# Kernel tuning notes

Hardware: AMD Instinct MI355X
Metric: run time of the kernel (lower is better)

## Reference

```python
import jax, jax.numpy as jnp
import numpy as np

N_EMBD = 1024
NUM_HEADS = 16
HEAD_SIZE = 64
B, T, T_ENC = 2, 2048, 2048


def setup_inputs() -> dict:
    key = jax.random.key(0)
    k1, k2, k3, k4, k5 = jax.random.split(key, 5)
    scale = 1.0 / np.sqrt(N_EMBD)
    return {
        "x_enc": jax.random.normal(k1, (B, T_ENC, N_EMBD), dtype=jnp.float32),
        "x": jax.random.normal(k2, (B, T, N_EMBD), dtype=jnp.float32),
        "Wk": jax.random.normal(k3, (N_EMBD, NUM_HEADS * HEAD_SIZE), dtype=jnp.float32) * scale,
        "Wq": jax.random.normal(k4, (N_EMBD, NUM_HEADS * HEAD_SIZE), dtype=jnp.float32) * scale,
        "Wv": jax.random.normal(k5, (N_EMBD, NUM_HEADS * HEAD_SIZE), dtype=jnp.float32) * scale,
    }


def reference(x_enc, x, Wk, Wq, Wv):
    b, t, c = x.shape
    _, t_enc, _ = x_enc.shape
    # projections (bias-free linears)
    k = (x_enc @ Wk).reshape(b, t_enc, NUM_HEADS, HEAD_SIZE)  # [B,S,H,D]
    v = (x_enc @ Wv).reshape(b, t_enc, NUM_HEADS, HEAD_SIZE)
    q = (x @ Wq).reshape(b, t, NUM_HEADS, HEAD_SIZE)          # [B,T,H,D]
    # NOTE: original scales by C**-0.5 with C = n_embd (not head_size)
    scale = jnp.asarray(c, x.dtype) ** -0.5
    wei = jnp.einsum("bthd,bshd->bhts", q, k) * scale          # [B,H,T,S]
    wei = jax.nn.softmax(wei, axis=-1)
    out = jnp.einsum("bhts,bshd->bthd", wei, v)                # [B,T,H,D]
    return out
```

## Files before the change

kernel.cpp:

```cpp
#include <hip/hip_runtime.h>
#include <hip/hip_bf16.h>
#include <stdint.h>

#define NE 1024
#define NH 16
#define HD 64
#define BB 2
#define TT 2048
#define MM (BB*TT)

typedef __attribute__((ext_vector_type(8))) short short8;
typedef __attribute__((ext_vector_type(4))) float floatx4;

__device__ __forceinline__ short f2bf(float f) {
    union { float f; uint32_t u; } v; v.f = f;
    uint32_t u = v.u;
    return (short)((u + 0x7fffu + ((u >> 16) & 1u)) >> 16);
}

__device__ __forceinline__ float fast_exp2(float x) {
#if __has_builtin(__builtin_amdgcn_exp2f)
    return __builtin_amdgcn_exp2f(x);
#else
    float r; asm("v_exp_f32 %0, %1" : "=v"(r) : "v"(x)); return r;
#endif
}

__device__ __forceinline__ void gload_lds16(const void* g, void* l) {
    __builtin_amdgcn_global_load_lds((__attribute__((address_space(1))) void*)g,
                                     (__attribute__((address_space(3))) void*)l,
                                     16, 0, 0);
}

__global__ void cvt_bf16(const float* __restrict__ in, short* __restrict__ out, int n8) {
    int i = blockIdx.x * blockDim.x + threadIdx.x;
    if (i >= n8) return;
    const floatx4* p = (const floatx4*)(in + (size_t)i * 8);
    floatx4 a = p[0], b = p[1];
    union { uint32_t u[4]; short8 s; } r;
    asm("v_cvt_pk_bf16_f32 %0, %1, %2" : "=v"(r.u[0]) : "v"(a[0]), "v"(a[1]));
    asm("v_cvt_pk_bf16_f32 %0, %1, %2" : "=v"(r.u[1]) : "v"(a[2]), "v"(a[3]));
    asm("v_cvt_pk_bf16_f32 %0, %1, %2" : "=v"(r.u[2]) : "v"(b[0]), "v"(b[1]));
    asm("v_cvt_pk_bf16_f32 %0, %1, %2" : "=v"(r.u[3]) : "v"(b[2]), "v"(b[3]));
    *(short8*)(out + (size_t)i * 8) = r.s;
}

__global__ void wtrans(const float* __restrict__ Wq, const float* __restrict__ Wk,
                       const float* __restrict__ Wv, short* __restrict__ Wt) {
    __shared__ float t[32][33];
    const float* W = blockIdx.z == 0 ? Wq : (blockIdx.z == 1 ? Wk : Wv);
    short* dst = Wt + (size_t)blockIdx.z * NE * NE;
    int n0 = blockIdx.x * 32, k0 = blockIdx.y * 32;
    int tx = threadIdx.x & 31, ty = threadIdx.x >> 5;
    #pragma unroll
    for (int i = 0; i < 4; i++)
        t[ty * 4 + i][tx] = W[(size_t)(k0 + ty * 4 + i) * NE + n0 + tx];
    __syncthreads();
    #pragma unroll
    for (int i = 0; i < 4; i++)
        dst[(size_t)(n0 + ty * 4 + i) * NE + k0 + tx] = f2bf(t[tx][ty * 4 + i]);
}

__global__ void __launch_bounds__(256) gemm_bt(const short* __restrict__ x_bf,
                                               const short* __restrict__ xenc_bf,
                                               const short* __restrict__ Wt,
                                               short* __restrict__ qkv) {
    __shared__ short sA[128 * 32];
    __shared__ short sB[128 * 32];
    const int z = blockIdx.z;
    const short* A  = (z == 0) ? x_bf : xenc_bf;
    const short* Bt = Wt + (size_t)z * NE * NE;
    short* C = qkv + (size_t)z * MM * NE;
    const float osc = (z == 0) ? 0.04508422f : 1.0f;

    const int tid = threadIdx.x;
    const int lane = tid & 63, wid = tid >> 6;
    const int l15 = lane & 15, lg = lane >> 4;
    const int wr = wid >> 1, wc = wid & 1;
    const int m0 = blockIdx.y * 128, n0 = blockIdx.x * 128;

    const short* gA = A  + (size_t)(m0 + (tid >> 2)) * NE + (tid & 3) * 8;
    const short* gB = Bt + (size_t)(n0 + (tid >> 2)) * NE + (tid & 3) * 8;
    short* lA = sA + wid * 512;
    short* lB = sB + wid * 512;

    floatx4 acc[4][4];
    floatx4 zero = {0.f, 0.f, 0.f, 0.f};
    #pragma unroll
    for (int i = 0; i < 4; i++)
        #pragma unroll
        for (int j = 0; j < 4; j++) acc[i][j] = zero;

    for (int kt = 0; kt < NE; kt += 32) {
        gload_lds16(gA + kt,            lA);
        gload_lds16(gA + 64 * NE + kt,  lA + 2048);
        gload_lds16(gB + kt,            lB);
        gload_lds16(gB + 64 * NE + kt,  lB + 2048);
        __syncthreads();
        short8 af[4], bfr[4];
        #pragma unroll
        for (int i = 0; i < 4; i++) {
            af[i]  = *(const short8*)&sA[(wr * 64 + i * 16 + l15) * 32 + lg * 8];
            bfr[i] = *(const short8*)&sB[(wc * 64 + i * 16 + l15) * 32 + lg * 8];
        }
        #pragma unroll
        for (int i = 0; i < 4; i++)
            #pragma unroll
            for (int j = 0; j < 4; j++)
                acc[i][j] = __builtin_amdgcn_mfma_f32_16x16x32_bf16(af[i], bfr[j], acc[i][j], 0, 0, 0);
        __syncthreads();
    }
    #pragma unroll
    for (int i = 0; i < 4; i++)
        #pragma unroll
        for (int j = 0; j < 4; j++)
            #pragma unroll
            for (int r = 0; r < 4; r++) {
                int row = m0 + wr * 64 + i * 16 + lg * 4 + r;
                int col = n0 + wc * 64 + j * 16 + l15;
                C[(size_t)row * NE + col] = f2bf(acc[i][j][r] * osc);
            }
}

__global__ void vtrans(const short* __restrict__ v, short* __restrict__ vt) {
    __shared__ short t[64][65];
    int s0 = blockIdx.x * 64;
    int bh = blockIdx.y;
    int b = bh >> 4, h = bh & 15;
    int tid = threadIdx.x;
    int c = tid & 63, rr = tid >> 6;
    #pragma unroll
    for (int i = 0; i < 16; i++)
        t[i * 4 + rr][c] = v[(size_t)(b * TT + s0 + i * 4 + rr) * NE + h * HD + c];
    __syncthreads();
    int csw = (c & 35) | (((c >> 4) & 1) << 2) | (((c >> 2) & 3) << 3);
    #pragma unroll
    for (int i = 0; i < 16; i++)
        vt[(size_t)(bh * HD + i * 4 + rr) * TT + s0 + csw] = t[c][i * 4 + rr];
}

__global__ void __launch_bounds__(256, 2) fattn(const short* __restrict__ q,
                                                const short* __restrict__ k,
                                                const short* __restrict__ vt,
                                                float* __restrict__ out) {
    __shared__ short kbuf[3][4096];
    __shared__ short vbuf[3][4096];
    const int tid = threadIdx.x, lane = tid & 63, wid = tid >> 6;
    const int l15 = lane & 15, lg = lane >> 4;
    const int q0 = blockIdx.x * 128 + wid * 32;
    const int bh = blockIdx.y, b = bh >> 4, h = bh & 15;

    short8 qf[2][2];
    #pragma unroll
    for (int qb = 0; qb < 2; qb++) {
        const short* qp = q + (size_t)(b * TT + q0 + qb * 16 + l15) * NE + h * HD + lg * 8;
        qf[qb][0] = *(const short8*)qp;
        qf[qb][1] = *(const short8*)(qp + 32);
    }
    short8 ones;
    #pragma unroll
    for (int j = 0; j < 8; j++) ones[j] = (short)0x3F80;

    floatx4 acc_o[2][4];
    floatx4 acc_l[2];
    floatx4 zero = {0.f, 0.f, 0.f, 0.f};
    floatx4 minus8 = {-8.f, -8.f, -8.f, -8.f};
    #pragma unroll
    for (int qb = 0; qb < 2; qb++) {
        acc_l[qb] = zero;
        #pragma unroll
        for (int db = 0; db < 4; db++) acc_o[qb][db] = zero;
    }

    const char* kgb = (const char*)(k + (size_t)(b * TT) * NE + h * HD);
    const char* vgb = (const char*)(vt + (size_t)bh * HD * TT);
    const int srow = tid >> 3;
    const int ssw  = ((tid & 7) * 16) ^ ((srow & 7) << 4);
    const char* ksrc = kgb + (size_t)srow * (NE * 2) + ssw;
    const char* vsrc = vgb + (size_t)srow * (TT * 2) + ssw;

    const int swz  = (l15 & 7) << 4;
    const int rd0  = l15 * 128 + ((lg * 16) ^ swz);
    const int rd1  = l15 * 128 + ((64 + lg * 16) ^ swz);

#define STAGE(bi, s0v) do { \
    const char* ks_ = ksrc + (size_t)(s0v) * (NE * 2); \
    gload_lds16(ks_,                 &kbuf[bi][wid * 512]); \
    gload_lds16(ks_ + 32 * (NE * 2), &kbuf[bi][wid * 512 + 2048]); \
    const char* vs_ = vsrc + (size_t)(s0v) * 2; \
    gload_lds16(vs_,                 &vbuf[bi][wid * 512]); \
    gload_lds16(vs_ + 32 * (TT * 2), &vbuf[bi][wid * 512 + 2048]); \
} while (0)

#define FATTN_COMPUTE(cur) do { \
    const char* kb = (const char*)kbuf[cur]; \
    const char* vb = (const char*)vbuf[cur]; \
    short8 kf[4][2]; \
    _Pragma("unroll") \
    for (int cb = 0; cb < 4; cb++) { \
        kf[cb][0] = *(const short8*)(kb + cb * 2048 + rd0); \
        kf[cb][1] = *(const short8*)(kb + cb * 2048 + rd1); \
    } \
    floatx4 sacc[2][4]; \
    _Pragma("unroll") \
    for (int qb = 0; qb < 2; qb++) \
        _Pragma("unroll") \
        for (int cb = 0; cb < 4; cb++) sacc[qb][cb] = minus8; \
    __builtin_amdgcn_s_setprio(1); \
    _Pragma("unroll") \
    for (int qb = 0; qb < 2; qb++) \
        _Pragma("unroll") \
        for (int cb = 0; cb < 4; cb++) { \
            sacc[qb][cb] = __builtin_amdgcn_mfma_f32_16x16x32_bf16(kf[cb][0], qf[qb][0], sacc[qb][cb], 0, 0, 0); \
            sacc[qb][cb] = __builtin_amdgcn_mfma_f32_16x16x32_bf16(kf[cb][1], qf[qb][1], sacc[qb][cb], 0, 0, 0); \
        } \
    __builtin_amdgcn_s_setprio(0); \
    short8 vf[2][4]; \
    _Pragma("unroll") \
    for (int db = 0; db < 4; db++) { \
        vf[0][db] = *(const short8*)(vb + db * 2048 + rd0); \
        vf[1][db] = *(const short8*)(vb + db * 2048 + rd1); \
    } \
    short8 paf[2][2]; \
    _Pragma("unroll") \
    for (int qb = 0; qb < 2; qb++) { \
        float pe[16]; \
        _Pragma("unroll") \
        for (int cb = 0; cb < 4; cb++) \
            _Pragma("unroll") \
            for (int r = 0; r < 4; r++) \
                pe[cb * 4 + r] = fast_exp2(sacc[qb][cb][r]); \
        _Pragma("unroll") \
        for (int ks = 0; ks < 2; ks++) { \
            union { uint32_t u[4]; short8 s; } pk_; \
            _Pragma("unroll") \
            for (int j2 = 0; j2 < 4; j2++) \
                asm("v_cvt_pk_bf16_f32 %0, %1, %2" \
                    : "=v"(pk_.u[j2]) \
                    : "v"(pe[ks * 8 + 2 * j2]), "v"(pe[ks * 8 + 2 * j2 + 1])); \
            paf[qb][ks] = pk_.s; \
        } \
    } \
    __builtin_amdgcn_s_setprio(1); \
    _Pragma("unroll") \
    for (int qb = 0; qb < 2; qb++) \
        _Pragma("unroll") \
        for (int ks = 0; ks < 2; ks++) { \
            _Pragma("unroll") \
            for (int db = 0; db < 4; db++) \
                acc_o[qb][db] = __builtin_amdgcn_mfma_f32_16x16x32_bf16(paf[qb][ks], vf[ks][db], acc_o[qb][db], 0, 0, 0); \
            acc_l[qb] = __builtin_amdgcn_mfma_f32_16x16x32_bf16(paf[qb][ks], ones, acc_l[qb], 0, 0, 0); \
        } \
    __builtin_amdgcn_s_setprio(0); \
} while (0)

    STAGE(0, 0);
    STAGE(1, 64);
    for (int t = 0; t < 31; ++t) {
        asm volatile("s_waitcnt vmcnt(4)" ::: "memory");
        __builtin_amdgcn_sched_barrier(0);
        __builtin_amdgcn_s_barrier();
        __builtin_amdgcn_sched_barrier(0);
        if (t < 30) STAGE((t + 2) % 3, (t + 2) * 64);
        FATTN_COMPUTE(t % 3);
    }
    asm volatile("s_waitcnt vmcnt(0)" ::: "memory");
    __builtin_amdgcn_sched_barrier(0);
    __builtin_amdgcn_s_barrier();
    __builtin_amdgcn_sched_barrier(0);
    FATTN_COMPUTE(1);
#undef STAGE
#undef FATTN_COMPUTE

    #pragma unroll
    for (int qb = 0; qb < 2; qb++) {
        #pragma unroll
        for (int r = 0; r < 4; r++) {
            float inv = 1.0f / acc_l[qb][r];
            #pragma unroll
            for (int db = 0; db < 4; db++)
                out[(size_t)(b * TT + q0 + qb * 16 + lg * 4 + r) * NE + h * HD + db * 16 + l15] =
                    acc_o[qb][db][r] * inv;
        }
    }
}

extern "C" void kernel_launch(void* const* d_in, const int* in_sizes, int n_in,
                              void* d_out, int out_size, void* d_ws, size_t ws_size,
                              hipStream_t stream) {
    const float* x_enc = (const float*)d_in[0];
    const float* x     = (const float*)d_in[1];
    const float* Wk    = (const float*)d_in[2];
    const float* Wq    = (const float*)d_in[3];
    const float* Wv    = (const float*)d_in[4];
    float* out = (float*)d_out;

    const size_t SZ = (size_t)MM * NE;
    short* x_bf    = (short*)d_ws;
    short* xenc_bf = x_bf + SZ;
    short* Wt      = xenc_bf + SZ;
    short* qkv     = Wt + 3 * (size_t)NE * NE;
    short* vt      = qkv + 3 * SZ;

    cvt_bf16<<<dim3(2048), dim3(256), 0, stream>>>(x,     x_bf,    (int)(SZ / 8));
    cvt_bf16<<<dim3(2048), dim3(256), 0, stream>>>(x_enc, xenc_bf, (int)(SZ / 8));
    wtrans<<<dim3(32, 32, 3), dim3(256), 0, stream>>>(Wq, Wk, Wv, Wt);
    gemm_bt<<<dim3(8, 32, 3), dim3(256), 0, stream>>>(x_bf, xenc_bf, Wt, qkv);
    vtrans<<<dim3(32, 32), dim3(256), 0, stream>>>(qkv + 2 * SZ, vt);
    fattn<<<dim3(16, 32), dim3(256), 0, stream>>>(qkv, qkv + SZ, vt, out);
}
```

Baseline: 101.6 us.

## Pipeline GEMM with triple-buffered LDS, XCD-aware block mapping, register-prefetch V in attention

Merges the two bf16 conversion kernels into one launch. Gives the projection GEMM a triple-buffered LDS pipeline that loads asynchronously to LDS, raises MFMA priority, and remaps 1D block ids so that neighbouring tiles share an XCD. The attention kernel gets the same XCD-aware remap, drops the V LDS staging in favour of direct global-to-register double-buffered V loads, and prefetches the next K fragments from LDS into registers. The aim is to overlap memory with MFMA work and improve L2 locality, at the cost of more registers and a full vmcnt(0) wait each iteration.

```diff
diff --git a/kernel.cpp b/kernel.cpp
--- a/kernel.cpp
+++ b/kernel.cpp
@@ -32,17 +32,20 @@
                                      16, 0, 0);
 }
 
-__global__ void cvt_bf16(const float* __restrict__ in, short* __restrict__ out, int n8) {
+__global__ void cvt_bf16_2(const float* __restrict__ ina, const float* __restrict__ inb,
+                           short* __restrict__ outa, short* __restrict__ outb, int n8half) {
     int i = blockIdx.x * blockDim.x + threadIdx.x;
-    if (i >= n8) return;
-    const floatx4* p = (const floatx4*)(in + (size_t)i * 8);
+    const float* in; short* out; int j;
+    if (i < n8half) { in = ina; out = outa; j = i; }
+    else            { in = inb; out = outb; j = i - n8half; }
+    const floatx4* p = (const floatx4*)(in + (size_t)j * 8);
     floatx4 a = p[0], b = p[1];
     union { uint32_t u[4]; short8 s; } r;
     asm("v_cvt_pk_bf16_f32 %0, %1, %2" : "=v"(r.u[0]) : "v"(a[0]), "v"(a[1]));
     asm("v_cvt_pk_bf16_f32 %0, %1, %2" : "=v"(r.u[1]) : "v"(a[2]), "v"(a[3]));
     asm("v_cvt_pk_bf16_f32 %0, %1, %2" : "=v"(r.u[2]) : "v"(b[0]), "v"(b[1]));
     asm("v_cvt_pk_bf16_f32 %0, %1, %2" : "=v"(r.u[3]) : "v"(b[2]), "v"(b[3]));
-    *(short8*)(out + (size_t)i * 8) = r.s;
+    *(short8*)(out + (size_t)j * 8) = r.s;
 }
 
 __global__ void wtrans(const float* __restrict__ Wq, const float* __restrict__ Wk,
@@ -65,9 +68,15 @@
                                                const short* __restrict__ xenc_bf,
                                                const short* __restrict__ Wt,
                                                short* __restrict__ qkv) {
-    __shared__ short sA[128 * 32];
-    __shared__ short sB[128 * 32];
-    const int z = blockIdx.z;
+    __shared__ short sA[3][4096];
+    __shared__ short sB[3][4096];
+    const int bid = blockIdx.x;
+    const int xcd = bid & 7, inner = bid >> 3;
+    const int xblk = inner & 7;
+    const int yh = (inner >> 3) & 3;
+    const int z = inner >> 5;
+    const int yblk = xcd + 8 * yh;
+
     const short* A  = (z == 0) ? x_bf : xenc_bf;
     const short* Bt = Wt + (size_t)z * NE * NE;
     short* C = qkv + (size_t)z * MM * NE;
@@ -77,12 +86,10 @@
     const int lane = tid & 63, wid = tid >> 6;
     const int l15 = lane & 15, lg = lane >> 4;
     const int wr = wid >> 1, wc = wid & 1;
-    const int m0 = blockIdx.y * 128, n0 = blockIdx.x * 128;
+    const int m0 = yblk * 128, n0 = xblk * 128;
 
     const short* gA = A  + (size_t)(m0 + (tid >> 2)) * NE + (tid & 3) * 8;
     const short* gB = Bt + (size_t)(n0 + (tid >> 2)) * NE + (tid & 3) * 8;
-    short* lA = sA + wid * 512;
-    short* lB = sB + wid * 512;
 
     floatx4 acc[4][4];
     floatx4 zero = {0.f, 0.f, 0.f, 0.f};
@@ -91,25 +98,47 @@
         #pragma unroll
         for (int j = 0; j < 4; j++) acc[i][j] = zero;
 
-    for (int kt = 0; kt < NE; kt += 32) {
-        gload_lds16(gA + kt,            lA);
-        gload_lds16(gA + 64 * NE + kt,  lA + 2048);
-        gload_lds16(gB + kt,            lB);
-        gload_lds16(gB + 64 * NE + kt,  lB + 2048);
-        __syncthreads();
-        short8 af[4], bfr[4];
-        #pragma unroll
-        for (int i = 0; i < 4; i++) {
-            af[i]  = *(const short8*)&sA[(wr * 64 + i * 16 + l15) * 32 + lg * 8];
-            bfr[i] = *(const short8*)&sB[(wc * 64 + i * 16 + l15) * 32 + lg * 8];
-        }
-        #pragma unroll
-        for (int i = 0; i < 4; i++)
-            #pragma unroll
-            for (int j = 0; j < 4; j++)
-                acc[i][j] = __builtin_amdgcn_mfma_f32_16x16x32_bf16(af[i], bfr[j], acc[i][j], 0, 0, 0);
-        __syncthreads();
-    }
+#define GSTAGE(bi, kt) do { \
+    gload_lds16(gA + (kt),            &sA[bi][wid * 512]); \
+    gload_lds16(gA + 64 * NE + (kt),  &sA[bi][wid * 512 + 2048]); \
+    gload_lds16(gB + (kt),            &sB[bi][wid * 512]); \
+    gload_lds16(gB + 64 * NE + (kt),  &sB[bi][wid * 512 + 2048]); \
+} while (0)
+
+#define GCOMP(cur) do { \
+    short8 af[4], bfr[4]; \
+    _Pragma("unroll") \
+    for (int i = 0; i < 4; i++) { \
+        af[i]  = *(const short8*)&sA[cur][(wr * 64 + i * 16 + l15) * 32 + lg * 8]; \
+        bfr[i] = *(const short8*)&sB[cur][(wc * 64 + i * 16 + l15) * 32 + lg * 8]; \
+    } \
+    __builtin_amdgcn_s_setprio(1); \
+    _Pragma("unroll") \
+    for (int i = 0; i < 4; i++) \
+        _Pragma("unroll") \
+        for (int j = 0; j < 4; j++) \
+            acc[i][j] = __builtin_amdgcn_mfma_f32_16x16x32_bf16(af[i], bfr[j], acc[i][j], 0, 0, 0); \
+    __builtin_amdgcn_s_setprio(0); \
+} while (0)
+
+    GSTAGE(0, 0);
+    GSTAGE(1, 32);
+    for (int t = 0; t < 31; ++t) {
+        asm volatile("s_waitcnt vmcnt(4)" ::: "memory");
+        __builtin_amdgcn_sched_barrier(0);
+        __builtin_amdgcn_s_barrier();
+        __builtin_amdgcn_sched_barrier(0);
+        if (t < 30) GSTAGE((t + 2) % 3, (t + 2) * 32);
+        GCOMP(t % 3);
+    }
+    asm volatile("s_waitcnt vmcnt(0)" ::: "memory");
+    __builtin_amdgcn_sched_barrier(0);
+    __builtin_amdgcn_s_barrier();
+    __builtin_amdgcn_sched_barrier(0);
+    GCOMP(1);
+#undef GSTAGE
+#undef GCOMP
+
     #pragma unroll
     for (int i = 0; i < 4; i++)
         #pragma unroll
@@ -144,11 +173,14 @@
                                                 const short* __restrict__ vt,
                                                 float* __restrict__ out) {
     __shared__ short kbuf[3][4096];
-    __shared__ short vbuf[3][4096];
     const int tid = threadIdx.x, lane = tid & 63, wid = tid >> 6;
     const int l15 = lane & 15, lg = lane >> 4;
-    const int q0 = blockIdx.x * 128 + wid * 32;
-    const int bh = blockIdx.y, b = bh >> 4, h = bh & 15;
+    const int bid = blockIdx.x;
+    const int xcd = bid & 7, rest = bid >> 3;
+    const int qblk = rest & 15;
+    const int bh = xcd + 8 * (rest >> 4);
+    const int b = bh >> 4, h = bh & 15;
+    const int q0 = qblk * 128 + wid * 32;
 
     short8 qf[2][2];
     #pragma unroll
@@ -173,34 +205,36 @@
     }
 
     const char* kgb = (const char*)(k + (size_t)(b * TT) * NE + h * HD);
-    const char* vgb = (const char*)(vt + (size_t)bh * HD * TT);
     const int srow = tid >> 3;
     const int ssw  = ((tid & 7) * 16) ^ ((srow & 7) << 4);
     const char* ksrc = kgb + (size_t)srow * (NE * 2) + ssw;
-    const char* vsrc = vgb + (size_t)srow * (TT * 2) + ssw;
+    const short* vrow = vt + (size_t)(bh * HD + l15) * TT + lg * 8;
 
     const int swz  = (l15 & 7) << 4;
     const int rd0  = l15 * 128 + ((lg * 16) ^ swz);
     const int rd1  = l15 * 128 + ((64 + lg * 16) ^ swz);
 
-#define STAGE(bi, s0v) do { \
+#define KSTAGE(bi, s0v) do { \
     const char* ks_ = ksrc + (size_t)(s0v) * (NE * 2); \
     gload_lds16(ks_,                 &kbuf[bi][wid * 512]); \
     gload_lds16(ks_ + 32 * (NE * 2), &kbuf[bi][wid * 512 + 2048]); \
-    const char* vs_ = vsrc + (size_t)(s0v) * 2; \
-    gload_lds16(vs_,                 &vbuf[bi][wid * 512]); \
-    gload_lds16(vs_ + 32 * (TT * 2), &vbuf[bi][wid * 512 + 2048]); \
-} while (0)
-
-#define FATTN_COMPUTE(cur) do { \
-    const char* kb = (const char*)kbuf[cur]; \
-    const char* vb = (const char*)vbuf[cur]; \
-    short8 kf[4][2]; \
-    _Pragma("unroll") \
-    for (int cb = 0; cb < 4; cb++) { \
-        kf[cb][0] = *(const short8*)(kb + cb * 2048 + rd0); \
-        kf[cb][1] = *(const short8*)(kb + cb * 2048 + rd1); \
+} while (0)
+
+#define VLOAD(vreg, s0v) do { \
+    const short* vp_ = vrow + (s0v); \
+    _Pragma("unroll") \
+    for (int db = 0; db < 4; db++) { \
+        vreg[0][db] = *(const short8*)(vp_ + (size_t)db * (16 * TT)); \
+        vreg[1][db] = *(const short8*)(vp_ + (size_t)db * (16 * TT) + 32); \
     } \
+} while (0)
+
+#define BODY(t, VCUR, VNXT) do { \
+    asm volatile("s_waitcnt vmcnt(0)" ::: "memory"); \
+    __builtin_amdgcn_sched_barrier(0); \
+    __builtin_amdgcn_s_barrier(); \
+    __builtin_amdgcn_sched_barrier(0); \
+    if ((t) < 30) KSTAGE(((t) + 2) % 3, ((t) + 2) * 64); \
     floatx4 sacc[2][4]; \
     _Pragma("unroll") \
     for (int qb = 0; qb < 2; qb++) \
@@ -211,15 +245,18 @@
     for (int qb = 0; qb < 2; qb++) \
         _Pragma("unroll") \
         for (int cb = 0; cb < 4; cb++) { \
-            sacc[qb][cb] = __builtin_amdgcn_mfma_f32_16x16x32_bf16(kf[cb][0], qf[qb][0], sacc[qb][cb], 0, 0, 0); \
-            sacc[qb][cb] = __builtin_amdgcn_mfma_f32_16x16x32_bf16(kf[cb][1], qf[qb][1], sacc[qb][cb], 0, 0, 0); \
+            sacc[qb][cb] = __builtin_amdgcn_mfma_f32_16x16x32_bf16(kfr[cb][0], qf[qb][0], sacc[qb][cb], 0, 0, 0); \
+            sacc[qb][cb] = __builtin_amdgcn_mfma_f32_16x16x32_bf16(kfr[cb][1], qf[qb][1], sacc[qb][cb], 0, 0, 0); \
         } \
     __builtin_amdgcn_s_setprio(0); \
-    short8 vf[2][4]; \
-    _Pragma("unroll") \
-    for (int db = 0; db < 4; db++) { \
-        vf[0][db] = *(const short8*)(vb + db * 2048 + rd0); \
-        vf[1][db] = *(const short8*)(vb + db * 2048 + rd1); \
+    if ((t) < 31) VLOAD(VNXT, ((t) + 1) * 64); \
+    if ((t) < 31) { \
+        const char* kb_ = (const char*)kbuf[((t) + 1) % 3]; \
+        _Pragma("unroll") \
+        for (int cb = 0; cb < 4; cb++) { \
+            kfr[cb][0] = *(const short8*)(kb_ + cb * 2048 + rd0); \
+            kfr[cb][1] = *(const short8*)(kb_ + cb * 2048 + rd1); \
+        } \
     } \
     short8 paf[2][2]; \
     _Pragma("unroll") \
@@ -248,29 +285,38 @@
         for (int ks = 0; ks < 2; ks++) { \
             _Pragma("unroll") \
             for (int db = 0; db < 4; db++) \
-                acc_o[qb][db] = __builtin_amdgcn_mfma_f32_16x16x32_bf16(paf[qb][ks], vf[ks][db], acc_o[qb][db], 0, 0, 0); \
+                acc_o[qb][db] = __builtin_amdgcn_mfma_f32_16x16x32_bf16(paf[qb][ks], VCUR[ks][db], acc_o[qb][db], 0, 0, 0); \
             acc_l[qb] = __builtin_amdgcn_mfma_f32_16x16x32_bf16(paf[qb][ks], ones, acc_l[qb], 0, 0, 0); \
         } \
     __builtin_amdgcn_s_setprio(0); \
 } while (0)
 
-    STAGE(0, 0);
-    STAGE(1, 64);
-    for (int t = 0; t < 31; ++t) {
-        asm volatile("s_waitcnt vmcnt(4)" ::: "memory");
-        __builtin_amdgcn_sched_barrier(0);
-        __builtin_amdgcn_s_barrier();
-        __builtin_amdgcn_sched_barrier(0);
-        if (t < 30) STAGE((t + 2) % 3, (t + 2) * 64);
-        FATTN_COMPUTE(t % 3);
-    }
+    short8 vfa[2][4], vfb[2][4];
+    short8 kfr[4][2];
+
+    KSTAGE(0, 0);
+    KSTAGE(1, 64);
+    VLOAD(vfa, 0);
     asm volatile("s_waitcnt vmcnt(0)" ::: "memory");
     __builtin_amdgcn_sched_barrier(0);
     __builtin_amdgcn_s_barrier();
     __builtin_amdgcn_sched_barrier(0);
-    FATTN_COMPUTE(1);
-#undef STAGE
-#undef FATTN_COMPUTE
+    {
+        const char* kb_ = (const char*)kbuf[0];
+        #pragma unroll
+        for (int cb = 0; cb < 4; cb++) {
+            kfr[cb][0] = *(const short8*)(kb_ + cb * 2048 + rd0);
+            kfr[cb][1] = *(const short8*)(kb_ + cb * 2048 + rd1);
+        }
+    }
+
+    for (int t = 0; t < 32; t += 2) {
+        BODY(t,     vfa, vfb);
+        BODY(t + 1, vfb, vfa);
+    }
+#undef BODY
+#undef VLOAD
+#undef KSTAGE
 
     #pragma unroll
     for (int qb = 0; qb < 2; qb++) {
@@ -302,10 +348,9 @@
     short* qkv     = Wt + 3 * (size_t)NE * NE;
     short* vt      = qkv + 3 * SZ;
 
-    cvt_bf16<<<dim3(2048), dim3(256), 0, stream>>>(x,     x_bf,    (int)(SZ / 8));
-    cvt_bf16<<<dim3(2048), dim3(256), 0, stream>>>(x_enc, xenc_bf, (int)(SZ / 8));
+    cvt_bf16_2<<<dim3(4096), dim3(256), 0, stream>>>(x, x_enc, x_bf, xenc_bf, (int)(SZ / 8));
     wtrans<<<dim3(32, 32, 3), dim3(256), 0, stream>>>(Wq, Wk, Wv, Wt);
-    gemm_bt<<<dim3(8, 32, 3), dim3(256), 0, stream>>>(x_bf, xenc_bf, Wt, qkv);
+    gemm_bt<<<dim3(768), dim3(256), 0, stream>>>(x_bf, xenc_bf, Wt, qkv);
     vtrans<<<dim3(32, 32), dim3(256), 0, stream>>>(qkv + 2 * SZ, vt);
-    fattn<<<dim3(16, 32), dim3(256), 0, stream>>>(qkv, qkv + SZ, vt, out);
-}
+    fattn<<<dim3(512), dim3(256), 0, stream>>>(qkv, qkv + SZ, vt, out);
+}
```

Measured after the change: 126.5 us. +24.6%, slower.
